# Kernel tuning notes

Hardware: AMD Instinct MI355X
Metric: run time of the kernel (lower is better)

The kernel has to match this reference:

```python
import jax, jax.numpy as jnp
import numpy as np

D_MODEL = 1024
NUM_HEADS = 16
HEAD_DIM = D_MODEL // NUM_HEADS  # 64
THETA = 10000.0
B, S = 2, 2048


def setup_inputs() -> dict:
    key = jax.random.key(0)
    k1, k2, k3 = jax.random.split(key, 3)
    sigma_qkv = (2.0 / (D_MODEL + 3 * D_MODEL)) ** 0.5
    sigma_o = (2.0 / (D_MODEL + D_MODEL)) ** 0.5
    x = jax.random.normal(k1, (B, S, D_MODEL), dtype=jnp.float32)
    w_qkv = jax.random.normal(k2, (3 * D_MODEL, D_MODEL), dtype=jnp.float32) * sigma_qkv
    w_o = jax.random.normal(k3, (D_MODEL, D_MODEL), dtype=jnp.float32) * sigma_o
    token_positions = jnp.arange(S, dtype=jnp.int32)
    return {"x": x, "w_qkv": w_qkv, "w_o": w_o, "token_positions": token_positions, "mask": 1}


def _rope(t, pos):
    # t: (B, H, S, HEAD_DIM); pos: (S,) int
    ids = jnp.arange(HEAD_DIM // 2, dtype=jnp.float32)
    freqs = pos.astype(jnp.float32)[:, None] * (THETA ** (-2.0 * ids / HEAD_DIM))  # (S, HEAD_DIM/2)
    cos, sin = jnp.cos(freqs), jnp.sin(freqs)
    even, odd = t[..., 0::2], t[..., 1::2]
    r_even = even * cos - odd * sin
    r_odd = odd * cos + even * sin
    # interleave back to original layout
    return jnp.stack([r_even, r_odd], axis=-1).reshape(t.shape)


def reference(x, w_qkv, w_o, token_positions, mask):
    # fused QKV projection: Linear computes x @ W^T with W [out, in]
    qkv = x @ w_qkv.T  # (B, S, 3*D_MODEL)
    q, k, v = jnp.split(qkv, 3, axis=-1)

    def to_heads(t):
        return t.reshape(B, S, NUM_HEADS, HEAD_DIM).transpose(0, 2, 1, 3)  # (B, H, S, Dh)

    q, k, v = to_heads(q), to_heads(k), to_heads(v)
    q = _rope(q, token_positions)
    k = _rope(k, token_positions)

    scores = jnp.einsum('bhqd,bhkd->bhqk', q, k)
    if mask:  # causal: lower-triangular allowed
        causal = jnp.tril(jnp.ones((S, S), dtype=bool))
        scores = jnp.where(causal, scores, -jnp.inf)
    attn = jax.nn.softmax(scores * (HEAD_DIM ** -0.5), axis=-1)
    out = jnp.einsum('bhqk,bhkd->bhqd', attn, v)  # (B, H, S, Dh)
    out = out.transpose(0, 2, 1, 3).reshape(B, S, D_MODEL)
    return out @ w_o.T
```

## Files before the change

### kernel.cpp

```cpp
#include <hip/hip_runtime.h>
#include <hip/hip_bf16.h>
#include <math.h>

typedef __bf16 bf16_t;
typedef __bf16 bf16x8 __attribute__((ext_vector_type(8)));
typedef __bf16 bf16x4 __attribute__((ext_vector_type(4)));
typedef float  f32x4  __attribute__((ext_vector_type(4)));
typedef float  f32x16 __attribute__((ext_vector_type(16)));

#define D_MODEL 1024
#define NH      16
#define HD      64
#define BATCH   2
#define SEQ     2048
#define MROWS   (BATCH*SEQ)
#define QKVN    (3*D_MODEL)
#define FA_PAD  72
#define SCALE_LOG2E 0.18033688011112042f

__device__ __forceinline__ void async_cp16(const bf16_t* g, bf16_t* l) {
    __builtin_amdgcn_global_load_lds(
        (const __attribute__((address_space(1))) void*)g,
        (__attribute__((address_space(3))) void*)l,
        16, 0, 0);
}

__device__ __forceinline__ float fexp2(float x) {
    float r;
    asm("v_exp_f32 %0, %1" : "=v"(r) : "v"(x));
    return r;
}

__device__ __forceinline__ unsigned cvtpk(float lo, float hi_) {
    unsigned r;
    asm("v_cvt_pk_bf16_f32 %0, %1, %2" : "=v"(r) : "v"(lo), "v"(hi_));
    return r;
}

__global__ void cvt_all(const float* __restrict__ x, const float* __restrict__ wq,
                        const float* __restrict__ wo,
                        bf16_t* __restrict__ xb, bf16_t* __restrict__ wqb,
                        bf16_t* __restrict__ wob) {
    const int nx = MROWS * D_MODEL, nq = QKVN * D_MODEL;
    int i = (blockIdx.x * blockDim.x + threadIdx.x) * 4;
    const float* s; bf16_t* d; int off;
    if (i < nx)           { s = x;  d = xb;  off = i; }
    else if (i < nx + nq) { s = wq; d = wqb; off = i - nx; }
    else                  { s = wo; d = wob; off = i - nx - nq; }
    float4 v = *(const float4*)(s + off);
    d[off]     = (bf16_t)v.x;
    d[off + 1] = (bf16_t)v.y;
    d[off + 2] = (bf16_t)v.z;
    d[off + 3] = (bf16_t)v.w;
}

template <typename OutT, int NI>
__global__ __launch_bounds__(256) void gemm_nt(const bf16_t* __restrict__ A,
                                               const bf16_t* __restrict__ Bm,
                                               OutT* __restrict__ C,
                                               int M, int N, int K) {
    __shared__ __align__(16) bf16_t AsA[128 * 32], AsB[128 * 32];
    __shared__ __align__(16) bf16_t BsA[NI * 32 * 32], BsB[NI * 32 * 32];
    const int tid  = threadIdx.x;
    const int w    = tid >> 6;
    const int lane = tid & 63;
    const int quad = lane >> 4;
    const int l16  = lane & 15;
    const int m0   = blockIdx.x * 128;
    const int n0   = blockIdx.y * (NI * 32);
    const int wm   = (w >> 1) * 64;
    const int wn   = (w & 1) * (NI * 16);

    f32x4 acc[4][NI];
    #pragma unroll
    for (int i = 0; i < 4; i++)
        #pragma unroll
        for (int j = 0; j < NI; j++)
            acc[i][j] = (f32x4){0.f, 0.f, 0.f, 0.f};

    const bf16_t* Ag0 = A  + (size_t)(m0 + (tid >> 2)) * K + (tid & 3) * 8;
    const bf16_t* Ag1 = Ag0 + (size_t)64 * K;
    const bf16_t* Bg0 = Bm + (size_t)(n0 + (tid >> 2)) * K + (tid & 3) * 8;
    const bf16_t* Bg1 = Bg0 + (size_t)64 * K;

    for (int k0 = 0; k0 < K; k0 += 64) {
        async_cp16(Ag0 + k0,      &AsA[(size_t)tid * 8]);
        async_cp16(Ag1 + k0,      &AsA[((size_t)tid + 256) * 8]);
        async_cp16(Ag0 + k0 + 32, &AsB[(size_t)tid * 8]);
        async_cp16(Ag1 + k0 + 32, &AsB[((size_t)tid + 256) * 8]);
        async_cp16(Bg0 + k0,      &BsA[(size_t)tid * 8]);
        async_cp16(Bg0 + k0 + 32, &BsB[(size_t)tid * 8]);
        if (NI == 4) {
            async_cp16(Bg1 + k0,      &BsA[((size_t)tid + 256) * 8]);
            async_cp16(Bg1 + k0 + 32, &BsB[((size_t)tid + 256) * 8]);
        }
        __syncthreads();

        bf16x8 af[4][2], bfr[NI][2];
        #pragma unroll
        for (int mi = 0; mi < 4; mi++) {
            af[mi][0] = *(const bf16x8*)&AsA[(wm + mi * 16 + l16) * 32 + quad * 8];
            af[mi][1] = *(const bf16x8*)&AsB[(wm + mi * 16 + l16) * 32 + quad * 8];
        }
        #pragma unroll
        for (int ni = 0; ni < NI; ni++) {
            bfr[ni][0] = *(const bf16x8*)&BsA[(wn + ni * 16 + l16) * 32 + quad * 8];
            bfr[ni][1] = *(const bf16x8*)&BsB[(wn + ni * 16 + l16) * 32 + quad * 8];
        }
        #pragma unroll
        for (int mi = 0; mi < 4; mi++)
            #pragma unroll
            for (int ni = 0; ni < NI; ni++) {
                acc[mi][ni] = __builtin_amdgcn_mfma_f32_16x16x32_bf16(
                    af[mi][0], bfr[ni][0], acc[mi][ni], 0, 0, 0);
                acc[mi][ni] = __builtin_amdgcn_mfma_f32_16x16x32_bf16(
                    af[mi][1], bfr[ni][1], acc[mi][ni], 0, 0, 0);
            }
        __syncthreads();
    }

    #pragma unroll
    for (int mi = 0; mi < 4; mi++)
        #pragma unroll
        for (int ni = 0; ni < NI; ni++) {
            const int col = n0 + wn + ni * 16 + l16;
            #pragma unroll
            for (int r = 0; r < 4; r++) {
                const int row = m0 + wm + mi * 16 + quad * 4 + r;
                C[(size_t)row * N + col] = (OutT)acc[mi][ni][r];
            }
        }
}

__global__ __launch_bounds__(256) void rope_split(const bf16_t* __restrict__ qkv,
                                                  const int* __restrict__ pos,
                                                  bf16_t* __restrict__ Qh,
                                                  bf16_t* __restrict__ Kh,
                                                  bf16_t* __restrict__ VT) {
    __shared__ bf16_t vs[128][FA_PAD];
    const int tid   = threadIdx.x;
    const int s_loc = tid >> 1;
    const int half  = tid & 1;
    const int s0    = blockIdx.x * 128;
    const int bh    = blockIdx.y;
    const int b     = bh >> 4, h = bh & 15;
    const int s     = s0 + s_loc;

    const bf16_t* row = qkv + (size_t)(b * SEQ + s) * QKVN + h * HD + half * 32;

    bf16_t qbuf[32], kbuf[32], vbuf[32];
    #pragma unroll
    for (int j = 0; j < 4; j++) {
        *(bf16x8*)&qbuf[j * 8] = *(const bf16x8*)(row + j * 8);
        *(bf16x8*)&kbuf[j * 8] = *(const bf16x8*)(row + D_MODEL + j * 8);
        *(bf16x8*)&vbuf[j * 8] = *(const bf16x8*)(row + 2 * D_MODEL + j * 8);
    }

    const float pf = (float)pos[s];
    #pragma unroll
    for (int p = 0; p < 16; p++) {
        const int d2 = half * 16 + p;
        const float inv = __expf(-0.28782313662425575f * (float)d2);
        const float f = pf * inv;
        const float c = cosf(f), sn = sinf(f);
        float qe = (float)qbuf[2 * p], qo = (float)qbuf[2 * p + 1];
        float ke = (float)kbuf[2 * p], ko = (float)kbuf[2 * p + 1];
        qbuf[2 * p]     = (bf16_t)((qe * c - qo * sn) * SCALE_LOG2E);
        qbuf[2 * p + 1] = (bf16_t)((qo * c + qe * sn) * SCALE_LOG2E);
        kbuf[2 * p]     = (bf16_t)(ke * c - ko * sn);
        kbuf[2 * p + 1] = (bf16_t)(ko * c + ke * sn);
    }

    bf16_t* qdst = Qh + ((size_t)bh * SEQ + s) * HD + half * 32;
    bf16_t* kdst = Kh + ((size_t)bh * SEQ + s) * HD + half * 32;
    #pragma unroll
    for (int j = 0; j < 4; j++) {
        *(bf16x8*)(qdst + j * 8) = *(bf16x8*)&qbuf[j * 8];
        *(bf16x8*)(kdst + j * 8) = *(bf16x8*)&kbuf[j * 8];
        *(bf16x8*)&vs[s_loc][half * 32 + j * 8] = *(bf16x8*)&vbuf[j * 8];
    }
    __syncthreads();

    const int d  = tid >> 2;
    const int sc = tid & 3;
    bf16_t tmp[32];
    #pragma unroll
    for (int i = 0; i < 32; i++) tmp[i] = vs[sc * 32 + i][d];
    bf16_t* vdst = VT + ((size_t)bh * HD + d) * SEQ + s0 + sc * 32;
    #pragma unroll
    for (int j = 0; j < 4; j++)
        *(bf16x8*)(vdst + j * 8) = *(bf16x8*)&tmp[j * 8];
}

__global__ __launch_bounds__(256) void flash_attn(const bf16_t* __restrict__ Qh,
                                                  const bf16_t* __restrict__ Kh,
                                                  const bf16_t* __restrict__ VT,
                                                  bf16_t* __restrict__ AO) {
    __shared__ __align__(16) bf16_t smem[4 * 64 * FA_PAD];
    bf16_t* Ks0 = smem;
    bf16_t* Vs0 = smem + 2 * 64 * FA_PAD;
    const int BUF = 64 * FA_PAD;

    const int tid  = threadIdx.x;
    const int w    = tid >> 6;
    const int lane = tid & 63;
    const int l31  = lane & 31;
    const int hi   = lane >> 5;
    const int qh   = w & 1;
    const int kh   = w >> 1;

    const int bid  = blockIdx.x;
    const int bh   = bid & 31;
    const int my_t = 31 - (bid >> 5);
    const int nkv  = my_t + 1;

    const bf16_t* Qb = Qh + (size_t)bh * SEQ * HD;
    const bf16_t* Kb = Kh + (size_t)bh * SEQ * HD;
    const bf16_t* Vb = VT + (size_t)bh * HD * SEQ;

    const int q0b = my_t * 64;
    const int qlo = q0b + qh * 32;
    const int qg  = qlo + l31;

    bf16x8 aq[4];
    #pragma unroll
    for (int ks = 0; ks < 4; ks++)
        aq[ks] = *(const bf16x8*)(Qb + (size_t)qg * HD + ks * 16 + hi * 8);

    const int srow = tid >> 3, scol = (tid & 7) * 8;
    const int lds0 = srow * FA_PAD + scol;
    const int lds1 = (srow + 32) * FA_PAD + scol;

    f32x16 o[2];
    #pragma unroll
    for (int dt = 0; dt < 2; dt++)
        #pragma unroll
        for (int i = 0; i < 16; i++) o[dt][i] = 0.f;
    float ls = 0.f;

    bf16x8 pK0 = *(const bf16x8*)(Kb + (size_t)srow * HD + scol);
    bf16x8 pK1 = *(const bf16x8*)(Kb + (size_t)(srow + 32) * HD + scol);
    bf16x8 pV0 = *(const bf16x8*)(Vb + (size_t)srow * SEQ + scol);
    bf16x8 pV1 = *(const bf16x8*)(Vb + (size_t)(srow + 32) * SEQ + scol);
    *(bf16x8*)&Ks0[lds0] = pK0;
    *(bf16x8*)&Ks0[lds1] = pK1;
    *(bf16x8*)&Vs0[lds0] = pV0;
    *(bf16x8*)&Vs0[lds1] = pV1;

    for (int kt = 0; kt < nkv; ++kt) {
        const int cur = kt & 1;
        __syncthreads();

        if (kt + 1 < nkv) {
            const int kn = (kt + 1) * 64;
            pK0 = *(const bf16x8*)(Kb + (size_t)(kn + srow) * HD + scol);
            pK1 = *(const bf16x8*)(Kb + (size_t)(kn + srow + 32) * HD + scol);
            pV0 = *(const bf16x8*)(Vb + (size_t)srow * SEQ + kn + scol);
            pV1 = *(const bf16x8*)(Vb + (size_t)(srow + 32) * SEQ + kn + scol);
        }

        const bf16_t* KsC = Ks0 + cur * BUF;
        const bf16_t* VsC = Vs0 + cur * BUF;
        const int kvbw = kt * 64 + kh * 32;
        if (kvbw <= qlo + 31) {
            const bool full = (kvbw + 31 <= qlo);

            bf16x8 kb[4];
            #pragma unroll
            for (int ks = 0; ks < 4; ks++)
                kb[ks] = *(const bf16x8*)&KsC[(kh * 32 + l31) * FA_PAD + ks * 16 + hi * 8];
            f32x16 t;
            #pragma unroll
            for (int i = 0; i < 16; i++) t[i] = 0.f;
            #pragma unroll
            for (int ks = 0; ks < 4; ks++)
                t = __builtin_amdgcn_mfma_f32_32x32x16_bf16(kb[ks], aq[ks], t, 0, 0, 0);

            float pv[16];
            #pragma unroll
            for (int r = 0; r < 16; r++) {
                float p = fexp2(t[r]);
                if (!full) {
                    const int kvg = kvbw + (r & 3) + 8 * (r >> 2) + 4 * hi;
                    if (kvg > qg) p = 0.f;
                }
                pv[r] = p;
            }
            ls += ((((pv[0] + pv[1]) + (pv[2] + pv[3]))
                  + ((pv[4] + pv[5]) + (pv[6] + pv[7])))
                 + (((pv[8] + pv[9]) + (pv[10] + pv[11]))
                  + ((pv[12] + pv[13]) + (pv[14] + pv[15]))));

            union { unsigned u[4]; bf16x8 v; } pa0, pa1;
            {
                unsigned a0 = cvtpk(pv[0], pv[1]);
                unsigned b0 = cvtpk(pv[4], pv[5]);
                unsigned a1 = cvtpk(pv[2], pv[3]);
                unsigned b1 = cvtpk(pv[6], pv[7]);
                asm volatile("v_permlane32_swap_b32 %0, %1" : "+v"(a0), "+v"(b0));
                asm volatile("v_permlane32_swap_b32 %0, %1" : "+v"(a1), "+v"(b1));
                pa0.u[0] = a0; pa0.u[1] = a1; pa0.u[2] = b0; pa0.u[3] = b1;
            }
            {
                unsigned a0 = cvtpk(pv[8], pv[9]);
                unsigned b0 = cvtpk(pv[12], pv[13]);
                unsigned a1 = cvtpk(pv[10], pv[11]);
                unsigned b1 = cvtpk(pv[14], pv[15]);
                asm volatile("v_permlane32_swap_b32 %0, %1" : "+v"(a0), "+v"(b0));
                asm volatile("v_permlane32_swap_b32 %0, %1" : "+v"(a1), "+v"(b1));
                pa1.u[0] = a0; pa1.u[1] = a1; pa1.u[2] = b0; pa1.u[3] = b1;
            }

            #pragma unroll
            for (int dt = 0; dt < 2; dt++) {
                const int vbase = (dt * 32 + l31) * FA_PAD + kh * 32 + hi * 8;
                bf16x8 vf0 = *(const bf16x8*)&VsC[vbase];
                bf16x8 vf1 = *(const bf16x8*)&VsC[vbase + 16];
                o[dt] = __builtin_amdgcn_mfma_f32_32x32x16_bf16(pa0.v, vf0, o[dt], 0, 0, 0);
                o[dt] = __builtin_amdgcn_mfma_f32_32x32x16_bf16(pa1.v, vf1, o[dt], 0, 0, 0);
            }
        }

        if (kt + 1 < nkv) {
            bf16_t* KsN = Ks0 + (cur ^ 1) * BUF;
            bf16_t* VsN = Vs0 + (cur ^ 1) * BUF;
            *(bf16x8*)&KsN[lds0] = pK0;
            *(bf16x8*)&KsN[lds1] = pK1;
            *(bf16x8*)&VsN[lds0] = pV0;
            *(bf16x8*)&VsN[lds1] = pV1;
        }
    }

    __syncthreads();
    ls += __shfl_xor(ls, 32);
    float* mrgO = (float*)smem;
    float* lsp  = mrgO + 2 * 32 * 66;
    if (kh == 1) {
        #pragma unroll
        for (int r = 0; r < 16; r++) {
            const int qlc = (r & 3) + 8 * (r >> 2) + 4 * hi;
            #pragma unroll
            for (int dt = 0; dt < 2; dt++)
                mrgO[(qh * 32 + qlc) * 66 + dt * 32 + l31] = o[dt][r];
        }
        if (hi == 0) lsp[qh * 32 + l31] = ls;
    }
    __syncthreads();
    if (kh == 0) {
        const float lt = ls + lsp[qh * 32 + l31];
        const int b = bh >> 4, hh = bh & 15;
        #pragma unroll
        for (int r = 0; r < 16; r++) {
            const int qlc = (r & 3) + 8 * (r >> 2) + 4 * hi;
            const float li = 1.0f / __shfl(lt, qlc);
            const size_t row = (size_t)b * SEQ + q0b + qh * 32 + qlc;
            #pragma unroll
            for (int dt = 0; dt < 2; dt++) {
                const float v = o[dt][r] + mrgO[(qh * 32 + qlc) * 66 + dt * 32 + l31];
                AO[row * D_MODEL + hh * HD + dt * 32 + l31] = (bf16_t)(v * li);
            }
        }
    }
}

extern "C" void kernel_launch(void* const* d_in, const int* in_sizes, int n_in,
                              void* d_out, int out_size, void* d_ws, size_t ws_size,
                              hipStream_t stream) {
    const float* x     = (const float*)d_in[0];
    const float* w_qkv = (const float*)d_in[1];
    const float* w_o   = (const float*)d_in[2];
    const int*   tpos  = (const int*)d_in[3];
    float*       out   = (float*)d_out;

    char* ws = (char*)d_ws;
    bf16_t* xb  = (bf16_t*)(ws);
    bf16_t* wqb = (bf16_t*)(ws + 8388608);
    bf16_t* wob = (bf16_t*)(ws + 14680064);
    bf16_t* qkv = (bf16_t*)(ws + 16777216);
    bf16_t* Qh  = (bf16_t*)(ws + 41943040);
    bf16_t* Kh  = (bf16_t*)(ws + 50331648);
    bf16_t* VT  = (bf16_t*)(ws + 58720256);
    bf16_t* AO  = (bf16_t*)(ws + 67108864);

    cvt_all<<<8192, 256, 0, stream>>>(x, w_qkv, w_o, xb, wqb, wob);

    gemm_nt<bf16_t, 4><<<dim3(32, 24), 256, 0, stream>>>(xb, wqb, qkv, MROWS, QKVN, D_MODEL);

    rope_split<<<dim3(SEQ / 128, BATCH * NH), 256, 0, stream>>>(qkv, tpos, Qh, Kh, VT);

    flash_attn<<<1024, 256, 0, stream>>>(Qh, Kh, VT, AO);

    gemm_nt<float, 2><<<dim3(32, 16), 256, 0, stream>>>(AO, wob, out, MROWS, D_MODEL, D_MODEL);
}
```

Baseline: 183.9 us.

## Split long causal query tiles across two KV halves with a merge kernel

The 16 longest causal query tiles per head are now split into two blocks that each process half of the KV range. Each half writes unnormalized fp32 partial outputs and row sums into a scratch buffer that reuses the qkv workspace, and a new fa_merge kernel adds the halves and normalizes into AO. The goal is better load balance and more blocks to fill the GPU during the tail of the attention kernel. The cost is an extra launch plus an fp32 partial write and read round trip. The merge is correct without max rescaling only because the kernel already uses a softmax with no running max.

```diff
diff --git a/kernel.cpp b/kernel.cpp
--- a/kernel.cpp
+++ b/kernel.cpp
@@ -195,7 +195,9 @@
 __global__ __launch_bounds__(256) void flash_attn(const bf16_t* __restrict__ Qh,
                                                   const bf16_t* __restrict__ Kh,
                                                   const bf16_t* __restrict__ VT,
-                                                  bf16_t* __restrict__ AO) {
+                                                  bf16_t* __restrict__ AO,
+                                                  float* __restrict__ Part,
+                                                  float* __restrict__ Lpart) {
     __shared__ __align__(16) bf16_t smem[4 * 64 * FA_PAD];
     bf16_t* Ks0 = smem;
     bf16_t* Vs0 = smem + 2 * 64 * FA_PAD;
@@ -211,8 +213,12 @@
 
     const int bid  = blockIdx.x;
     const int bh   = bid & 31;
-    const int my_t = 31 - (bid >> 5);
-    const int nkv  = my_t + 1;
+    const int unit = bid >> 5;
+
+    int my_t, k0i, k1i, half;
+    if (unit < 16)      { my_t = 31 - unit;        half = 0;  k0i = 0;               k1i = (my_t + 1) >> 1; }
+    else if (unit < 32) { my_t = 31 - (unit - 16); half = 1;  k0i = (my_t + 1) >> 1; k1i = my_t + 1; }
+    else                { my_t = 47 - unit;        half = -1; k0i = 0;               k1i = my_t + 1; }
 
     const bf16_t* Qb = Qh + (size_t)bh * SEQ * HD;
     const bf16_t* Kb = Kh + (size_t)bh * SEQ * HD;
@@ -238,20 +244,21 @@
         for (int i = 0; i < 16; i++) o[dt][i] = 0.f;
     float ls = 0.f;
 
-    bf16x8 pK0 = *(const bf16x8*)(Kb + (size_t)srow * HD + scol);
-    bf16x8 pK1 = *(const bf16x8*)(Kb + (size_t)(srow + 32) * HD + scol);
-    bf16x8 pV0 = *(const bf16x8*)(Vb + (size_t)srow * SEQ + scol);
-    bf16x8 pV1 = *(const bf16x8*)(Vb + (size_t)(srow + 32) * SEQ + scol);
+    const int kn0 = k0i * 64;
+    bf16x8 pK0 = *(const bf16x8*)(Kb + (size_t)(kn0 + srow) * HD + scol);
+    bf16x8 pK1 = *(const bf16x8*)(Kb + (size_t)(kn0 + srow + 32) * HD + scol);
+    bf16x8 pV0 = *(const bf16x8*)(Vb + (size_t)srow * SEQ + kn0 + scol);
+    bf16x8 pV1 = *(const bf16x8*)(Vb + (size_t)(srow + 32) * SEQ + kn0 + scol);
     *(bf16x8*)&Ks0[lds0] = pK0;
     *(bf16x8*)&Ks0[lds1] = pK1;
     *(bf16x8*)&Vs0[lds0] = pV0;
     *(bf16x8*)&Vs0[lds1] = pV1;
 
-    for (int kt = 0; kt < nkv; ++kt) {
-        const int cur = kt & 1;
+    for (int kt = k0i; kt < k1i; ++kt) {
+        const int cur = (kt - k0i) & 1;
         __syncthreads();
 
-        if (kt + 1 < nkv) {
+        if (kt + 1 < k1i) {
             const int kn = (kt + 1) * 64;
             pK0 = *(const bf16x8*)(Kb + (size_t)(kn + srow) * HD + scol);
             pK1 = *(const bf16x8*)(Kb + (size_t)(kn + srow + 32) * HD + scol);
@@ -321,7 +328,7 @@
             }
         }
 
-        if (kt + 1 < nkv) {
+        if (kt + 1 < k1i) {
             bf16_t* KsN = Ks0 + (cur ^ 1) * BUF;
             bf16_t* VsN = Vs0 + (cur ^ 1) * BUF;
             *(bf16x8*)&KsN[lds0] = pK0;
@@ -348,19 +355,62 @@
     __syncthreads();
     if (kh == 0) {
         const float lt = ls + lsp[qh * 32 + l31];
-        const int b = bh >> 4, hh = bh & 15;
-        #pragma unroll
-        for (int r = 0; r < 16; r++) {
-            const int qlc = (r & 3) + 8 * (r >> 2) + 4 * hi;
-            const float li = 1.0f / __shfl(lt, qlc);
-            const size_t row = (size_t)b * SEQ + q0b + qh * 32 + qlc;
-            #pragma unroll
-            for (int dt = 0; dt < 2; dt++) {
-                const float v = o[dt][r] + mrgO[(qh * 32 + qlc) * 66 + dt * 32 + l31];
-                AO[row * D_MODEL + hh * HD + dt * 32 + l31] = (bf16_t)(v * li);
-            }
-        }
-    }
+        if (half < 0) {
+            const int b = bh >> 4, hh = bh & 15;
+            #pragma unroll
+            for (int r = 0; r < 16; r++) {
+                const int qlc = (r & 3) + 8 * (r >> 2) + 4 * hi;
+                const float li = 1.0f / __shfl(lt, qlc);
+                const size_t row = (size_t)b * SEQ + q0b + qh * 32 + qlc;
+                #pragma unroll
+                for (int dt = 0; dt < 2; dt++) {
+                    const float v = o[dt][r] + mrgO[(qh * 32 + qlc) * 66 + dt * 32 + l31];
+                    AO[row * D_MODEL + hh * HD + dt * 32 + l31] = (bf16_t)(v * li);
+                }
+            }
+        } else {
+            const int sidx = (bh * 16 + (my_t - 16)) * 2 + half;
+            float* po = Part + (size_t)sidx * 4096;
+            #pragma unroll
+            for (int r = 0; r < 16; r++) {
+                const int qlc = (r & 3) + 8 * (r >> 2) + 4 * hi;
+                const int q = qh * 32 + qlc;
+                #pragma unroll
+                for (int dt = 0; dt < 2; dt++)
+                    po[q * 64 + dt * 32 + l31] =
+                        o[dt][r] + mrgO[(qh * 32 + qlc) * 66 + dt * 32 + l31];
+            }
+            if (hi == 0) Lpart[(size_t)sidx * 64 + qh * 32 + l31] = lt;
+        }
+    }
+}
+
+__global__ __launch_bounds__(256) void fa_merge(const float* __restrict__ Part,
+                                                const float* __restrict__ Lpart,
+                                                bf16_t* __restrict__ AO) {
+    const int bid = blockIdx.x;
+    const int bh  = bid & 31;
+    const int ti  = bid >> 5;
+    const int t   = 16 + ti;
+    const int sidx = (bh * 16 + ti) * 2;
+    const float* p0 = Part + (size_t)sidx * 4096;
+    const float* p1 = p0 + 4096;
+    const float* l0 = Lpart + (size_t)sidx * 64;
+    const float* l1 = l0 + 64;
+
+    const int tid = threadIdx.x;
+    const int q   = tid >> 2;
+    const int dg  = (tid & 3) * 16;
+    const float li = 1.0f / (l0[q] + l1[q]);
+    const int b = bh >> 4, hh = bh & 15;
+
+    bf16_t outv[16];
+    #pragma unroll
+    for (int j = 0; j < 16; j++)
+        outv[j] = (bf16_t)((p0[q * 64 + dg + j] + p1[q * 64 + dg + j]) * li);
+    bf16_t* dst = AO + ((size_t)b * SEQ + t * 64 + q) * D_MODEL + hh * HD + dg;
+    *(bf16x8*)dst       = *(bf16x8*)&outv[0];
+    *(bf16x8*)(dst + 8) = *(bf16x8*)&outv[8];
 }
 
 extern "C" void kernel_launch(void* const* d_in, const int* in_sizes, int n_in,
@@ -381,6 +431,8 @@
     bf16_t* Kh  = (bf16_t*)(ws + 50331648);
     bf16_t* VT  = (bf16_t*)(ws + 58720256);
     bf16_t* AO  = (bf16_t*)(ws + 67108864);
+    float*  Part  = (float*)(ws + 16777216);
+    float*  Lpart = Part + 32 * 16 * 2 * 4096;
 
     cvt_all<<<8192, 256, 0, stream>>>(x, w_qkv, w_o, xb, wqb, wob);
 
@@ -388,7 +440,9 @@
 
     rope_split<<<dim3(SEQ / 128, BATCH * NH), 256, 0, stream>>>(qkv, tpos, Qh, Kh, VT);
 
-    flash_attn<<<1024, 256, 0, stream>>>(Qh, Kh, VT, AO);
+    flash_attn<<<1536, 256, 0, stream>>>(Qh, Kh, VT, AO, Part, Lpart);
+
+    fa_merge<<<512, 256, 0, stream>>>(Part, Lpart, AO);
 
     gemm_nt<float, 2><<<dim3(32, 16), 256, 0, stream>>>(AO, wob, out, MROWS, D_MODEL, D_MODEL);
 }
```

After: 190.5 us. 1.04x slower.
